# Kernel optimization log

Measured on AMD Instinct MI355X. Metric: run time of the kernel, lower is better.

The kernel has to match this reference:

```python
import jax, jax.numpy as jnp
import numpy as np

B, T, S, DM, H, HID = 4, 1024, 1024, 1024, 16, 4096
DEPTH = DM // H


def setup_inputs() -> dict:
    key = jax.random.key(0)
    ks = jax.random.split(key, 32)
    n = lambda k, shape, scale=1.0: jax.random.normal(k, shape, dtype=jnp.float32) * scale
    w_scale = 1.0 / np.sqrt(DM)
    inp = {
        "x": n(ks[0], (B, T, DM)),
        "enc_out": n(ks[1], (B, S, DM)),
        # causal mask: 1 where attention is forbidden (TF convention mask*-1e9)
        "look_ahead_mask": jnp.broadcast_to(
            jnp.triu(jnp.ones((T, T), jnp.float32), k=1), (B, 1, T, T)),
        "padding_mask": jnp.zeros((B, 1, 1, S), jnp.float32),
    }
    # self-attention MHA params
    names = ["wq1", "wk1", "wv1", "wo1", "wq2", "wk2", "wv2", "wo2"]
    for i, nm in enumerate(names):
        inp[nm] = n(ks[2 + i], (DM, DM), w_scale)
        inp["b" + nm[1:]] = jnp.zeros((DM,), jnp.float32)
    # FFN
    inp["wh"] = n(ks[10], (DM, HID), w_scale)
    inp["bh"] = jnp.zeros((HID,), jnp.float32)
    inp["wout"] = n(ks[11], (HID, DM), 1.0 / np.sqrt(HID))
    inp["bout"] = jnp.zeros((DM,), jnp.float32)
    for i in (1, 2, 3):
        inp[f"g{i}"] = jnp.ones((DM,), jnp.float32)
        inp[f"be{i}"] = jnp.zeros((DM,), jnp.float32)
    return inp


def _layer_norm(x, gamma, beta, eps=1e-6):
    mean = jnp.mean(x, axis=-1, keepdims=True)
    var = jnp.mean(jnp.square(x - mean), axis=-1, keepdims=True)
    return gamma * (x - mean) * jax.lax.rsqrt(var + eps) + beta


def _mha(q_in, k_in, v_in, mask, wq, bq, wk, bk, wv, bv, wo, bo):
    b = q_in.shape[0]
    split = lambda t: t.reshape(b, -1, H, DEPTH).transpose(0, 2, 1, 3)  # [b,h,s,d]
    Q = split(q_in @ wq + bq)
    K = split(k_in @ wk + bk)
    V = split(v_in @ wv + bv)
    scores = jnp.einsum("bhqd,bhkd->bhqk", Q, K) / jnp.sqrt(jnp.float32(DEPTH))
    scores = scores + mask * (-1e9)
    w = jax.nn.softmax(scores, axis=-1)
    out = jnp.einsum("bhqk,bhkd->bhqd", w, V)
    out = out.transpose(0, 2, 1, 3).reshape(b, -1, DM)
    return out @ wo + bo


def reference(x, enc_out, look_ahead_mask, padding_mask,
              wq1, bq1, wk1, bk1, wv1, bv1, wo1, bo1,
              wq2, bq2, wk2, bk2, wv2, bv2, wo2, bo2,
              wh, bh, wout, bout, g1, be1, g2, be2, g3, be3):
    # self-attention + residual + LN (dropout identity at inference)
    a1 = _mha(x, x, x, look_ahead_mask, wq1, bq1, wk1, bk1, wv1, bv1, wo1, bo1)
    h1 = _layer_norm(a1 + x, g1, be1)
    # cross-attention + residual + LN
    a2 = _mha(h1, enc_out, enc_out, padding_mask,
              wq2, bq2, wk2, bk2, wv2, bv2, wo2, bo2)
    h2 = _layer_norm(a2 + h1, g2, be2)
    # FFN + residual + LN
    f = jax.nn.relu(h2 @ wh + bh) @ wout + bout
    return _layer_norm(f + h2, g3, be3)
```

## Files before the change

### kernel.cpp

```cpp
#include <hip/hip_runtime.h>
#include <hip/hip_bf16.h>

typedef __bf16 bf16;
typedef __bf16 bf16x4 __attribute__((ext_vector_type(4)));
typedef __bf16 bf16x8 __attribute__((ext_vector_type(8)));
typedef float floatx4 __attribute__((ext_vector_type(4)));

#define MFMA16(a, b, c) __builtin_amdgcn_mfma_f32_16x16x32_bf16(a, b, c, 0, 0, 0)

#define BB   4
#define TT   1024
#define SS   1024
#define DMOD 1024
#define NH   16
#define DH   64
#define HID  4096
#define MTOT (BB * TT)

__device__ __forceinline__ float loadf(const bf16* p)  { return (float)*p; }
__device__ __forceinline__ float loadf(const float* p) { return *p; }

__device__ __forceinline__ void gll16(const bf16* g, bf16* l) {
    __builtin_amdgcn_global_load_lds(
        (const __attribute__((address_space(1))) void*)g,
        (__attribute__((address_space(3))) void*)l, 16, 0, 0);
}

__device__ __forceinline__ void xcd_swizzle2d(int& bx, int& by) {
    const int gx  = gridDim.x;
    const int nwg = gx * gridDim.y;
    const int lin = blockIdx.y * gx + blockIdx.x;
    const int q   = nwg >> 3;
    const int swz = (lin & 7) * q + (lin >> 3);
    bx = swz % gx;
    by = swz / gx;
}

struct TBatch { const float* src[8]; bf16* dst[8]; };

__global__ __launch_bounds__(256)
void transpose_sq_kernel(TBatch tb)
{
    __shared__ float t[64][65];
    const float* W = tb.src[blockIdx.z];
    bf16* WT = tb.dst[blockIdx.z];
    const int k0 = blockIdx.y * 64, n0 = blockIdx.x * 64;
    const int tid = threadIdx.x;
    const int r = tid >> 4, c = (tid & 15) * 4;
    #pragma unroll
    for (int i = 0; i < 4; ++i) {
        float4 v = *(const float4*)(W + (size_t)(k0 + i * 16 + r) * DMOD + n0 + c);
        t[i * 16 + r][c + 0] = v.x; t[i * 16 + r][c + 1] = v.y;
        t[i * 16 + r][c + 2] = v.z; t[i * 16 + r][c + 3] = v.w;
    }
    __syncthreads();
    #pragma unroll
    for (int i = 0; i < 4; ++i) {
        int n = i * 16 + r;
        bf16x4 o;
        #pragma unroll
        for (int j = 0; j < 4; ++j) o[j] = (bf16)t[c + j][n];
        *(bf16x4*)(WT + (size_t)(n0 + n) * DMOD + k0 + c) = o;
    }
}

__global__ __launch_bounds__(256)
void transpose_kernel(const float* __restrict__ W, bf16* __restrict__ WT, int K, int N)
{
    __shared__ float t[64][65];
    const int k0 = blockIdx.y * 64, n0 = blockIdx.x * 64;
    const int tid = threadIdx.x;
    const int r = tid >> 4, c = (tid & 15) * 4;
    #pragma unroll
    for (int i = 0; i < 4; ++i) {
        float4 v = *(const float4*)(W + (size_t)(k0 + i * 16 + r) * N + n0 + c);
        t[i * 16 + r][c + 0] = v.x; t[i * 16 + r][c + 1] = v.y;
        t[i * 16 + r][c + 2] = v.z; t[i * 16 + r][c + 3] = v.w;
    }
    __syncthreads();
    #pragma unroll
    for (int i = 0; i < 4; ++i) {
        int n = i * 16 + r;
        bf16x4 o;
        #pragma unroll
        for (int j = 0; j < 4; ++j) o[j] = (bf16)t[c + j][n];
        *(bf16x4*)(WT + (size_t)(n0 + n) * K + k0 + c) = o;
    }
}

__global__ __launch_bounds__(256)
void vtrans_kernel(const bf16* __restrict__ in, int ldi, bf16* __restrict__ out)
{
    __shared__ bf16 t[64][72];
    const int r0 = blockIdx.y * 64;
    const int c0 = blockIdx.x * 64;
    const int tid = threadIdx.x;
    const int rr = tid >> 3;
    const int c8 = (tid & 7) * 8;
    #pragma unroll
    for (int i = 0; i < 2; ++i) {
        int row = i * 32 + rr;
        bf16x8 v = *(const bf16x8*)(in + (size_t)(r0 + row) * ldi + c0 + c8);
        *(bf16x8*)(&t[row][c8]) = v;
    }
    __syncthreads();
    #pragma unroll
    for (int i = 0; i < 2; ++i) {
        int col = i * 32 + rr;
        bf16x8 v;
        #pragma unroll
        for (int j = 0; j < 8; ++j) v[j] = t[c8 + j][col];
        *(bf16x8*)(out + (size_t)(c0 + col) * MTOT + r0 + c8) = v;
    }
}

__global__ __launch_bounds__(256)
void cvt_kernel(const float* __restrict__ in, bf16* __restrict__ out, int n4)
{
    int i = blockIdx.x * 256 + threadIdx.x;
    if (i < n4) {
        float4 v = ((const float4*)in)[i];
        bf16x4 o = { (bf16)v.x, (bf16)v.y, (bf16)v.z, (bf16)v.w };
        ((bf16x4*)out)[i] = o;
    }
}

__global__ __launch_bounds__(256)
void bias_concat_kernel(const float* bq1, const float* bk1, const float* bv1,
                        const float* bk2, const float* bv2, float* __restrict__ biasc)
{
    int i = blockIdx.x * 256 + threadIdx.x;
    float v;
    if      (i < 1024) v = bq1[i];
    else if (i < 2048) v = bk1[i - 1024];
    else if (i < 3072) v = bv1[i - 2048];
    else if (i < 4096) v = bk2[i - 3072];
    else               v = bv2[i - 4096];
    if (i < 5120) biasc[i] = v;
}

template <int EPI, typename TR>
__global__ __launch_bounds__(256, 2)
void gemm_kernel(const bf16* __restrict__ A, int lda, const bf16* __restrict__ B,
                 const float* __restrict__ bias, const TR* __restrict__ resid,
                 bf16* __restrict__ out, int M, int N, int K)
{
    __shared__ bf16 Al[2][128 * 64];
    __shared__ bf16 Bl[2][128 * 64];

    const int tid  = threadIdx.x;
    const int wave = tid >> 6;
    const int lane = tid & 63;
    const int l16  = lane & 15;
    const int quad = lane >> 4;
    int bx, by;
    xcd_swizzle2d(bx, by);
    const int bm   = by * 128;
    const int bn   = bx * 128;
    const int wm   = (wave >> 1) * 64;
    const int wn   = (wave & 1) * 64;
    const int lrow = lane >> 3;
    const int scol = ((lane & 7) ^ lrow) * 8;

    floatx4 acc[4][4] = {};
    const int ntk = K / 64;

    auto STAGE = [&](int kt, int buf) {
        const int k0 = kt * 64;
        #pragma unroll
        for (int i = 0; i < 4; ++i) {
            int r0 = (wave * 4 + i) * 8;
            gll16(A + (size_t)(bm + r0 + lrow) * lda + k0 + scol, &Al[buf][r0 * 64]);
            gll16(B + (size_t)(bn + r0 + lrow) * K   + k0 + scol, &Bl[buf][r0 * 64]);
        }
    };

    auto COMPUTE = [&](int buf) {
        #pragma unroll
        for (int ks = 0; ks < 2; ++ks) {
            bf16x8 af[4], bg[4];
            const int xo = ((ks * 4 + quad) ^ (l16 & 7)) * 8;
            #pragma unroll
            for (int mt = 0; mt < 4; ++mt)
                af[mt] = *(const bf16x8*)(&Al[buf][(wm + mt * 16 + l16) * 64 + xo]);
            #pragma unroll
            for (int nt = 0; nt < 4; ++nt)
                bg[nt] = *(const bf16x8*)(&Bl[buf][(wn + nt * 16 + l16) * 64 + xo]);
            #pragma unroll
            for (int mt = 0; mt < 4; ++mt)
                #pragma unroll
                for (int nt = 0; nt < 4; ++nt)
                    acc[mt][nt] = MFMA16(af[mt], bg[nt], acc[mt][nt]);
        }
    };

    STAGE(0, 0);
    asm volatile("s_waitcnt vmcnt(0)" ::: "memory");
    __builtin_amdgcn_s_barrier();

    int cur = 0;
    for (int t = 0; t < ntk - 1; ++t) {
        STAGE(t + 1, cur ^ 1);
        COMPUTE(cur);
        asm volatile("s_waitcnt vmcnt(0) lgkmcnt(0)" ::: "memory");
        __builtin_amdgcn_s_barrier();
        cur ^= 1;
    }
    COMPUTE(cur);

    #pragma unroll
    for (int mt = 0; mt < 4; ++mt) {
        int row0 = bm + wm + mt * 16 + quad * 4;
        #pragma unroll
        for (int nt = 0; nt < 4; ++nt) {
            int col = bn + wn + nt * 16 + l16;
            float bv = bias[col];
            #pragma unroll
            for (int r = 0; r < 4; ++r) {
                float v = acc[mt][nt][r] + bv;
                size_t idx = (size_t)(row0 + r) * N + col;
                if (EPI == 1) v = fmaxf(v, 0.0f);
                if (EPI == 2) v += loadf(resid + idx);
                out[idx] = (bf16)v;
            }
        }
    }
}

template <int EPI, typename TR>
__global__ __launch_bounds__(256, 3)
void gemm64_kernel(const bf16* __restrict__ A, int lda, const bf16* __restrict__ B,
                   const float* __restrict__ bias, const TR* __restrict__ resid,
                   bf16* __restrict__ out, int M, int N, int K)
{
    __shared__ bf16 Al[2][64 * 64];
    __shared__ bf16 Bl[2][128 * 64];

    const int tid  = threadIdx.x;
    const int wave = tid >> 6;
    const int lane = tid & 63;
    const int l16  = lane & 15;
    const int quad = lane >> 4;
    int bx, by;
    xcd_swizzle2d(bx, by);
    const int bm   = by * 64;
    const int bn   = bx * 128;
    const int wm   = (wave >> 1) * 32;
    const int wn   = (wave & 1) * 64;
    const int lrow = lane >> 3;
    const int scol = ((lane & 7) ^ lrow) * 8;

    floatx4 acc[2][4] = {};
    const int ntk = K / 64;

    auto STAGE = [&](int kt, int buf) {
        const int k0 = kt * 64;
        #pragma unroll
        for (int i = 0; i < 2; ++i) {
            int r0 = wave * 16 + i * 8;
            gll16(A + (size_t)(bm + r0 + lrow) * lda + k0 + scol, &Al[buf][r0 * 64]);
        }
        #pragma unroll
        for (int i = 0; i < 4; ++i) {
            int r0 = (wave * 4 + i) * 8;
            gll16(B + (size_t)(bn + r0 + lrow) * K + k0 + scol, &Bl[buf][r0 * 64]);
        }
    };

    auto COMPUTE = [&](int buf) {
        #pragma unroll
        for (int ks = 0; ks < 2; ++ks) {
            bf16x8 af[2], bg[4];
            const int xo = ((ks * 4 + quad) ^ (l16 & 7)) * 8;
            #pragma unroll
            for (int mt = 0; mt < 2; ++mt)
                af[mt] = *(const bf16x8*)(&Al[buf][(wm + mt * 16 + l16) * 64 + xo]);
            #pragma unroll
            for (int nt = 0; nt < 4; ++nt)
                bg[nt] = *(const bf16x8*)(&Bl[buf][(wn + nt * 16 + l16) * 64 + xo]);
            #pragma unroll
            for (int mt = 0; mt < 2; ++mt)
                #pragma unroll
                for (int nt = 0; nt < 4; ++nt)
                    acc[mt][nt] = MFMA16(af[mt], bg[nt], acc[mt][nt]);
        }
    };

    STAGE(0, 0);
    asm volatile("s_waitcnt vmcnt(0)" ::: "memory");
    __builtin_amdgcn_s_barrier();

    int cur = 0;
    for (int t = 0; t < ntk - 1; ++t) {
        STAGE(t + 1, cur ^ 1);
        COMPUTE(cur);
        asm volatile("s_waitcnt vmcnt(0) lgkmcnt(0)" ::: "memory");
        __builtin_amdgcn_s_barrier();
        cur ^= 1;
    }
    COMPUTE(cur);

    #pragma unroll
    for (int mt = 0; mt < 2; ++mt) {
        int row0 = bm + wm + mt * 16 + quad * 4;
        #pragma unroll
        for (int nt = 0; nt < 4; ++nt) {
            int col = bn + wn + nt * 16 + l16;
            float bv = bias[col];
            #pragma unroll
            for (int r = 0; r < 4; ++r) {
                float v = acc[mt][nt][r] + bv;
                size_t idx = (size_t)(row0 + r) * N + col;
                if (EPI == 1) v = fmaxf(v, 0.0f);
                if (EPI == 2) v += loadf(resid + idx);
                out[idx] = (bf16)v;
            }
        }
    }
}

template <int CAUSAL>
__global__ __launch_bounds__(256, 3)
void attn_kernel(const bf16* __restrict__ Q, int ldq, const bf16* __restrict__ K, int ldk,
                 const bf16* __restrict__ Vt, bf16* __restrict__ O, int ldo)
{
    __shared__ bf16 Kl[2][64 * 64];
    __shared__ bf16 Vl[2][64 * 64];
    __shared__ bf16 Pl[4 * 16 * 72];

    const int tid  = threadIdx.x;
    const int wave = tid >> 6;
    const int lane = tid & 63;
    const int l16  = lane & 15;
    const int quad = lane >> 4;
    int bx, byy, bz;
    {
        const int lin = (blockIdx.z * 16 + blockIdx.y) * 16 + blockIdx.x;
        const int swz = (lin & 7) * 128 + (lin >> 3);
        bx  = swz & 15;
        byy = (swz >> 4) & 15;
        bz  = swz >> 8;
    }
    const int qb   = CAUSAL ? (15 - bx) : bx;
    const int h    = byy;
    const int b    = bz;

    const int qrow0 = b * TT + qb * 64 + wave * 16;
    const int colh  = h * DH;
    const int lr8   = lane >> 3;
    const int lc8s  = ((lane & 7) ^ lr8) * 8;

    bf16x8 qa[2];
    #pragma unroll
    for (int c = 0; c < 2; ++c)
        qa[c] = *(const bf16x8*)(Q + (size_t)(qrow0 + l16) * ldq + colh + c * 32 + quad * 8);

    floatx4 o[5] = {};
    const float C = 0.125f * 1.4426950408889634f;
    bf16x8 onesf;
    {
        bf16 ov = (bf16)((l16 == 0) ? 1.0f : 0.0f);
        #pragma unroll
        for (int j = 0; j < 8; ++j) onesf[j] = ov;
    }

    const int ntiles = CAUSAL ? qb + 1 : (SS / 64);
    bf16* pw = Pl + wave * (16 * 72);

    auto STAGE = [&](int t, int buf) {
        const int kv0 = t * 64;
        #pragma unroll
        for (int i = 0; i < 2; ++i) {
            int r0 = wave * 16 + i * 8;
            gll16(K  + (size_t)(b * SS + kv0 + r0 + lr8) * ldk + colh + lc8s, &Kl[buf][r0 * 64]);
            gll16(Vt + (size_t)(colh + r0 + lr8) * MTOT + b * SS + kv0 + lc8s, &Vl[buf][r0 * 64]);
        }
    };

    auto COMPUTE = [&](int t, int buf) {
        const int xo0 = (quad ^ (l16 & 7)) * 8;
        const int xo1 = ((4 + quad) ^ (l16 & 7)) * 8;

        floatx4 s[4];
        #pragma unroll
        for (int nt = 0; nt < 4; ++nt) {
            bf16x8 kb0 = *(const bf16x8*)(&Kl[buf][(nt * 16 + l16) * 64 + xo0]);
            bf16x8 kb1 = *(const bf16x8*)(&Kl[buf][(nt * 16 + l16) * 64 + xo1]);
            floatx4 z = {};
            z = MFMA16(qa[0], kb0, z);
            z = MFMA16(qa[1], kb1, z);
            s[nt] = z;
        }

        const bool dm = CAUSAL && (t == qb);
        #pragma unroll
        for (int nt = 0; nt < 4; ++nt)
            #pragma unroll
            for (int r = 0; r < 4; ++r) {
                float sv = s[nt][r] * C;
                if (dm) {
                    int qg  = wave * 16 + quad * 4 + r;
                    int kvg = nt * 16 + l16;
                    if (kvg > qg) sv = -1e30f;
                }
                float pv = exp2f(sv);
                pw[(quad * 4 + r) * 72 + nt * 16 + l16] = (bf16)pv;
            }

        bf16x8 pa0 = *(const bf16x8*)(pw + l16 * 72 + quad * 8);
        bf16x8 pa1 = *(const bf16x8*)(pw + l16 * 72 + 32 + quad * 8);
        #pragma unroll
        for (int dt = 0; dt < 4; ++dt) {
            bf16x8 vb0 = *(const bf16x8*)(&Vl[buf][(dt * 16 + l16) * 64 + xo0]);
            bf16x8 vb1 = *(const bf16x8*)(&Vl[buf][(dt * 16 + l16) * 64 + xo1]);
            o[dt] = MFMA16(pa0, vb0, o[dt]);
            o[dt] = MFMA16(pa1, vb1, o[dt]);
        }
        o[4] = MFMA16(pa0, onesf, o[4]);
        o[4] = MFMA16(pa1, onesf, o[4]);
    };

    STAGE(0, 0);
    asm volatile("s_waitcnt vmcnt(0)" ::: "memory");
    __builtin_amdgcn_s_barrier();

    int cur = 0;
    for (int t = 0; t < ntiles - 1; ++t) {
        STAGE(t + 1, cur ^ 1);
        COMPUTE(t, cur);
        asm volatile("s_waitcnt vmcnt(0) lgkmcnt(0)" ::: "memory");
        __builtin_amdgcn_s_barrier();
        cur ^= 1;
    }
    COMPUTE(ntiles - 1, cur);

    #pragma unroll
    for (int r = 0; r < 4; ++r) {
        float lr  = __shfl(o[4][r], (lane & 48));
        float inv = __builtin_amdgcn_rcpf(lr);
        #pragma unroll
        for (int dt = 0; dt < 4; ++dt) {
            float ov = o[dt][r] * inv;
            size_t idx = (size_t)(qrow0 + quad * 4 + r) * ldo + colh + dt * 16 + l16;
            O[idx] = (bf16)ov;
        }
    }
}

template <typename TO>
__global__ __launch_bounds__(256)
void ln_kernel(const bf16* __restrict__ in, const float* __restrict__ g,
               const float* __restrict__ be, TO* __restrict__ out)
{
    const int row = blockIdx.x;
    const int tid = threadIdx.x;
    bf16x4 xv = *(const bf16x4*)(in + (size_t)row * DMOD + tid * 4);
    float x0 = (float)xv[0], x1 = (float)xv[1], x2 = (float)xv[2], x3 = (float)xv[3];

    float s = x0 + x1 + x2 + x3;
    #pragma unroll
    for (int off = 32; off >= 1; off >>= 1) s += __shfl_xor(s, off);
    __shared__ float red1[4];
    __shared__ float red2[4];
    const int wave = tid >> 6;
    if ((tid & 63) == 0) red1[wave] = s;
    __syncthreads();
    float mean = (red1[0] + red1[1] + red1[2] + red1[3]) * (1.0f / DMOD);

    float d0 = x0 - mean, d1 = x1 - mean, d2 = x2 - mean, d3 = x3 - mean;
    float sq = d0 * d0 + d1 * d1 + d2 * d2 + d3 * d3;
    #pragma unroll
    for (int off = 32; off >= 1; off >>= 1) sq += __shfl_xor(sq, off);
    if ((tid & 63) == 0) red2[wave] = sq;
    __syncthreads();
    float var = (red2[0] + red2[1] + red2[2] + red2[3]) * (1.0f / DMOD);
    float rs = rsqrtf(var + 1e-6f);

    int c = tid * 4;
    size_t o0 = (size_t)row * DMOD + c;
    out[o0 + 0] = (TO)(g[c + 0] * d0 * rs + be[c + 0]);
    out[o0 + 1] = (TO)(g[c + 1] * d1 * rs + be[c + 1]);
    out[o0 + 2] = (TO)(g[c + 2] * d2 * rs + be[c + 2]);
    out[o0 + 3] = (TO)(g[c + 3] * d3 * rs + be[c + 3]);
}

extern "C" void kernel_launch(void* const* d_in, const int* in_sizes, int n_in,
                              void* d_out, int out_size, void* d_ws, size_t ws_size,
                              hipStream_t stream)
{
    const float* x   = (const float*)d_in[0];
    const float* enc = (const float*)d_in[1];
    const float* wq1 = (const float*)d_in[4];  const float* bq1 = (const float*)d_in[5];
    const float* wk1 = (const float*)d_in[6];  const float* bk1 = (const float*)d_in[7];
    const float* wv1 = (const float*)d_in[8];  const float* bv1 = (const float*)d_in[9];
    const float* wo1 = (const float*)d_in[10]; const float* bo1 = (const float*)d_in[11];
    const float* wq2 = (const float*)d_in[12]; const float* bq2 = (const float*)d_in[13];
    const float* wk2 = (const float*)d_in[14]; const float* bk2 = (const float*)d_in[15];
    const float* wv2 = (const float*)d_in[16]; const float* bv2 = (const float*)d_in[17];
    const float* wo2 = (const float*)d_in[18]; const float* bo2 = (const float*)d_in[19];
    const float* wh  = (const float*)d_in[20]; const float* bh  = (const float*)d_in[21];
    const float* wou = (const float*)d_in[22]; const float* bou = (const float*)d_in[23];
    const float* g1  = (const float*)d_in[24]; const float* be1 = (const float*)d_in[25];
    const float* g2  = (const float*)d_in[26]; const float* be2 = (const float*)d_in[27];
    const float* g3  = (const float*)d_in[28]; const float* be3 = (const float*)d_in[29];

    const int M = MTOT;
    const size_t MB = 1u << 20;
    dim3 blk(256);

    char* ws = (char*)d_ws;
    bf16*  WT    = (bf16*)(ws);
    float* biasc = (float*)(ws + 8 * MB);
    bf16*  xb    = (bf16*)(ws + 9 * MB);
    bf16*  h1    = (bf16*)(ws + 9 * MB);
    bf16*  tmpb3 = (bf16*)(ws + 9 * MB);
    bf16*  encb  = (bf16*)(ws + 17 * MB);
    bf16*  Vt2   = (bf16*)(ws + 17 * MB);
    bf16*  ffn   = (bf16*)(ws + 17 * MB);
    bf16*  qkv   = (bf16*)(ws + 25 * MB);
    bf16*  kvb   = qkv + (size_t)M * 1024;
    bf16*  tmpb2 = qkv + (size_t)M * 1024;
    bf16*  Vt1   = (bf16*)(ws + 49 * MB);
    bf16*  tmpb1 = (bf16*)(ws + 49 * MB);
    bf16*  h2    = (bf16*)(ws + 49 * MB);

    dim3 gThi(HID / 64, DMOD / 64);
    dim3 gTout(DMOD / 64, HID / 64);
    dim3 gVt(DMOD / 64, M / 64);
    dim3 gQKV(3072 / 128, M / 128);
    dim3 gKV(2048 / 128, M / 128);
    dim3 gN64(DMOD / 128, M / 64);
    dim3 gH(HID / 128, M / 128);
    dim3 gA(TT / 64, NH, BB);
    const size_t W1M = (size_t)1024 * 1024;

    cvt_kernel<<<dim3(M * DMOD / 4 / 256), blk, 0, stream>>>(x, xb, M * DMOD / 4);
    cvt_kernel<<<dim3(M * DMOD / 4 / 256), blk, 0, stream>>>(enc, encb, M * DMOD / 4);
    bias_concat_kernel<<<dim3(20), blk, 0, stream>>>(bq1, bk1, bv1, bk2, bv2, biasc);

    {
        TBatch tb;
        tb.src[0] = wq1; tb.dst[0] = WT + 0 * W1M;
        tb.src[1] = wk1; tb.dst[1] = WT + 1 * W1M;
        tb.src[2] = wv1; tb.dst[2] = WT + 2 * W1M;
        tb.src[3] = wo1; tb.dst[3] = WT + 3 * W1M;
        tb.src[4] = tb.src[5] = tb.src[6] = tb.src[7] = wq1;
        tb.dst[4] = tb.dst[5] = tb.dst[6] = tb.dst[7] = WT;
        dim3 g4(16, 16, 4);
        transpose_sq_kernel<<<g4, blk, 0, stream>>>(tb);
    }

    gemm_kernel<0, bf16><<<gQKV, blk, 0, stream>>>(xb, 1024, WT, biasc, (const bf16*)nullptr,
                                                   qkv, M, 3072, 1024);
    vtrans_kernel<<<gVt, blk, 0, stream>>>(qkv + 2048, 3072, Vt1);
    attn_kernel<1><<<gA, blk, 0, stream>>>(qkv, 3072, qkv + 1024, 3072, Vt1, qkv, 3072);
    gemm64_kernel<2, float><<<gN64, blk, 0, stream>>>(qkv, 3072, WT + 3 * W1M, bo1, x,
                                                      tmpb1, M, 1024, 1024);
    ln_kernel<bf16><<<dim3(M), blk, 0, stream>>>(tmpb1, g1, be1, h1);

    {
        TBatch tb;
        tb.src[0] = wq2; tb.dst[0] = WT + 0 * W1M;
        tb.src[1] = wk2; tb.dst[1] = WT + 1 * W1M;
        tb.src[2] = wv2; tb.dst[2] = WT + 2 * W1M;
        tb.src[3] = wo2; tb.dst[3] = WT + 3 * W1M;
        tb.src[4] = tb.src[5] = tb.src[6] = tb.src[7] = wq2;
        tb.dst[4] = tb.dst[5] = tb.dst[6] = tb.dst[7] = WT;
        dim3 g4(16, 16, 4);
        transpose_sq_kernel<<<g4, blk, 0, stream>>>(tb);
    }

    gemm64_kernel<0, bf16><<<gN64, blk, 0, stream>>>(h1, 1024, WT, bq2, (const bf16*)nullptr,
                                                     qkv, M, 1024, 1024);
    gemm_kernel<0, bf16><<<gKV, blk, 0, stream>>>(encb, 1024, WT + 1 * W1M, biasc + 3072,
                                                  (const bf16*)nullptr, kvb, M, 2048, 1024);
    vtrans_kernel<<<gVt, blk, 0, stream>>>(kvb + 1024, 2048, Vt2);
    attn_kernel<0><<<gA, blk, 0, stream>>>(qkv, 1024, kvb, 2048, Vt2, qkv, 1024);
    gemm64_kernel<2, bf16><<<gN64, blk, 0, stream>>>(qkv, 1024, WT + 3 * W1M, bo2, h1,
                                                     tmpb2, M, 1024, 1024);
    ln_kernel<bf16><<<dim3(M), blk, 0, stream>>>(tmpb2, g2, be2, h2);

    transpose_kernel<<<gThi, blk, 0, stream>>>(wh, WT, DMOD, HID);
    gemm_kernel<1, bf16><<<gH, blk, 0, stream>>>(h2, 1024, WT, bh, (const bf16*)nullptr,
                                                 ffn, M, HID, 1024);
    transpose_kernel<<<gTout, blk, 0, stream>>>(wou, WT, HID, DMOD);
    gemm64_kernel<2, bf16><<<gN64, blk, 0, stream>>>(ffn, 4096, WT, bou, h2,
                                                     tmpb3, M, 1024, 4096);
    ln_kernel<float><<<dim3(M), blk, 0, stream>>>(tmpb3, g3, be3, (float*)d_out);
}
```

Measured before the change: 521.8 us.

## Add 256x256-tile 8-wave GEMM with phased prefetch for wide-N projections

```diff
diff --git a/kernel.cpp b/kernel.cpp
--- a/kernel.cpp
+++ b/kernel.cpp
@@ -137,6 +137,155 @@
     else if (i < 4096) v = bk2[i - 3072];
     else               v = bv2[i - 4096];
     if (i < 5120) biasc[i] = v;
+}
+
+template <int EPI, typename TR>
+__global__ __launch_bounds__(512, 2)
+void gemm256_kernel(const bf16* __restrict__ A, int lda, const bf16* __restrict__ B,
+                    const float* __restrict__ bias, const TR* __restrict__ resid,
+                    bf16* __restrict__ out, int M, int N, int K)
+{
+    __shared__ bf16 Al[2][256 * 64];
+    __shared__ bf16 Bl[2][256 * 64];
+
+    const int tid  = threadIdx.x;
+    const int wave = tid >> 6;
+    const int lane = tid & 63;
+    const int l16  = lane & 15;
+    const int quad = lane >> 4;
+    const int wr   = wave >> 2;
+    const int wc   = wave & 3;
+    int bx, by;
+    xcd_swizzle2d(bx, by);
+    const int bm   = by * 256;
+    const int bn   = bx * 256;
+    const int lrow = lane >> 3;
+    const int scol = ((lane & 7) ^ lrow) * 8;
+
+    floatx4 acc[8][4] = {};
+    const int ntk = K / 64;
+
+    auto STAGE_A = [&](int kt, int half, int buf) {
+        const int k0 = kt * 64;
+        #pragma unroll
+        for (int i = 0; i < 2; ++i) {
+            int r0 = half * 128 + i * 64 + wave * 8;
+            gll16(A + (size_t)(bm + r0 + lrow) * lda + k0 + scol, &Al[buf][r0 * 64]);
+        }
+    };
+    auto STAGE_B = [&](int kt, int half, int buf) {
+        const int k0 = kt * 64;
+        #pragma unroll
+        for (int i = 0; i < 2; ++i) {
+            int r0 = half * 128 + i * 64 + wave * 8;
+            gll16(B + (size_t)(bn + r0 + lrow) * K + k0 + scol, &Bl[buf][r0 * 64]);
+        }
+    };
+
+    STAGE_A(0, 0, 0); STAGE_A(0, 1, 0); STAGE_B(0, 0, 0); STAGE_B(0, 1, 0);
+
+    for (int t = 0; t < ntk; ++t) {
+        const int buf = t & 1, nb = buf ^ 1;
+        const bool hn = (t + 1 < ntk);
+        bf16x8 bg[4], af[4];
+
+        if (hn) {
+            STAGE_A(t + 1, 0, nb);
+            asm volatile("s_waitcnt vmcnt(2)" ::: "memory");
+        } else {
+            asm volatile("s_waitcnt vmcnt(0)" ::: "memory");
+        }
+        __builtin_amdgcn_s_barrier();
+        {
+            const int xo = (quad ^ (l16 & 7)) * 8;
+            #pragma unroll
+            for (int i = 0; i < 4; ++i)
+                af[i] = *(const bf16x8*)(&Al[buf][(wr * 128 + i * 16 + l16) * 64 + xo]);
+            #pragma unroll
+            for (int n = 0; n < 4; ++n)
+                bg[n] = *(const bf16x8*)(&Bl[buf][(wc * 64 + n * 16 + l16) * 64 + xo]);
+        }
+        __builtin_amdgcn_s_setprio(1);
+        #pragma unroll
+        for (int i = 0; i < 4; ++i)
+            #pragma unroll
+            for (int n = 0; n < 4; ++n)
+                acc[i][n] = MFMA16(af[i], bg[n], acc[i][n]);
+        __builtin_amdgcn_s_setprio(0);
+        __builtin_amdgcn_s_barrier();
+
+        {
+            const int xo = (quad ^ (l16 & 7)) * 8;
+            #pragma unroll
+            for (int i = 0; i < 4; ++i)
+                af[i] = *(const bf16x8*)(&Al[buf][(wr * 128 + 64 + i * 16 + l16) * 64 + xo]);
+        }
+        if (hn) STAGE_A(t + 1, 1, nb);
+        __builtin_amdgcn_s_barrier();
+        __builtin_amdgcn_s_setprio(1);
+        #pragma unroll
+        for (int i = 0; i < 4; ++i)
+            #pragma unroll
+            for (int n = 0; n < 4; ++n)
+                acc[4 + i][n] = MFMA16(af[i], bg[n], acc[4 + i][n]);
+        __builtin_amdgcn_s_setprio(0);
+        __builtin_amdgcn_s_barrier();
+
+        {
+            const int xo = ((4 + quad) ^ (l16 & 7)) * 8;
+            #pragma unroll
+            for (int i = 0; i < 4; ++i)
+                af[i] = *(const bf16x8*)(&Al[buf][(wr * 128 + i * 16 + l16) * 64 + xo]);
+            #pragma unroll
+            for (int n = 0; n < 4; ++n)
+                bg[n] = *(const bf16x8*)(&Bl[buf][(wc * 64 + n * 16 + l16) * 64 + xo]);
+        }
+        if (hn) STAGE_B(t + 1, 0, nb);
+        __builtin_amdgcn_s_barrier();
+        __builtin_amdgcn_s_setprio(1);
+        #pragma unroll
+        for (int i = 0; i < 4; ++i)
+            #pragma unroll
+            for (int n = 0; n < 4; ++n)
+                acc[i][n] = MFMA16(af[i], bg[n], acc[i][n]);
+        __builtin_amdgcn_s_setprio(0);
+        __builtin_amdgcn_s_barrier();
+
+        {
+            const int xo = ((4 + quad) ^ (l16 & 7)) * 8;
+            #pragma unroll
+            for (int i = 0; i < 4; ++i)
+                af[i] = *(const bf16x8*)(&Al[buf][(wr * 128 + 64 + i * 16 + l16) * 64 + xo]);
+        }
+        if (hn) STAGE_B(t + 1, 1, nb);
+        __builtin_amdgcn_s_barrier();
+        __builtin_amdgcn_s_setprio(1);
+        #pragma unroll
+        for (int i = 0; i < 4; ++i)
+            #pragma unroll
+            for (int n = 0; n < 4; ++n)
+                acc[4 + i][n] = MFMA16(af[i], bg[n], acc[4 + i][n]);
+        __builtin_amdgcn_s_setprio(0);
+        __builtin_amdgcn_s_barrier();
+    }
+
+    #pragma unroll
+    for (int mf = 0; mf < 8; ++mf) {
+        int row0 = bm + wr * 128 + mf * 16 + quad * 4;
+        #pragma unroll
+        for (int nf = 0; nf < 4; ++nf) {
+            int col = bn + wc * 64 + nf * 16 + l16;
+            float bv = bias[col];
+            #pragma unroll
+            for (int r = 0; r < 4; ++r) {
+                float v = acc[mf][nf][r] + bv;
+                size_t idx = (size_t)(row0 + r) * N + col;
+                if (EPI == 1) v = fmaxf(v, 0.0f);
+                if (EPI == 2) v += loadf(resid + idx);
+                out[idx] = (bf16)v;
+            }
+        }
+    }
 }
 
 template <int EPI, typename TR>
@@ -228,7 +377,7 @@
 }
 
 template <int EPI, typename TR>
-__global__ __launch_bounds__(256, 3)
+__global__ __launch_bounds__(256, 2)
 void gemm64_kernel(const bf16* __restrict__ A, int lda, const bf16* __restrict__ B,
                    const float* __restrict__ bias, const TR* __restrict__ resid,
                    bf16* __restrict__ out, int M, int N, int K)
@@ -507,6 +656,7 @@
     const int M = MTOT;
     const size_t MB = 1u << 20;
     dim3 blk(256);
+    dim3 blk512(512);
 
     char* ws = (char*)d_ws;
     bf16*  WT    = (bf16*)(ws);
@@ -527,10 +677,10 @@
     dim3 gThi(HID / 64, DMOD / 64);
     dim3 gTout(DMOD / 64, HID / 64);
     dim3 gVt(DMOD / 64, M / 64);
-    dim3 gQKV(3072 / 128, M / 128);
-    dim3 gKV(2048 / 128, M / 128);
+    dim3 gQKV256(3072 / 256, M / 256);
+    dim3 gKV256(2048 / 256, M / 256);
+    dim3 gFFN1(HID / 256, M / 256);
     dim3 gN64(DMOD / 128, M / 64);
-    dim3 gH(HID / 128, M / 128);
     dim3 gA(TT / 64, NH, BB);
     const size_t W1M = (size_t)1024 * 1024;
 
@@ -550,8 +700,8 @@
         transpose_sq_kernel<<<g4, blk, 0, stream>>>(tb);
     }
 
-    gemm_kernel<0, bf16><<<gQKV, blk, 0, stream>>>(xb, 1024, WT, biasc, (const bf16*)nullptr,
-                                                   qkv, M, 3072, 1024);
+    gemm256_kernel<0, bf16><<<gQKV256, blk512, 0, stream>>>(xb, 1024, WT, biasc,
+                                                            (const bf16*)nullptr, qkv, M, 3072, 1024);
     vtrans_kernel<<<gVt, blk, 0, stream>>>(qkv + 2048, 3072, Vt1);
     attn_kernel<1><<<gA, blk, 0, stream>>>(qkv, 3072, qkv + 1024, 3072, Vt1, qkv, 3072);
     gemm64_kernel<2, float><<<gN64, blk, 0, stream>>>(qkv, 3072, WT + 3 * W1M, bo1, x,
@@ -572,8 +722,8 @@
 
     gemm64_kernel<0, bf16><<<gN64, blk, 0, stream>>>(h1, 1024, WT, bq2, (const bf16*)nullptr,
                                                      qkv, M, 1024, 1024);
-    gemm_kernel<0, bf16><<<gKV, blk, 0, stream>>>(encb, 1024, WT + 1 * W1M, biasc + 3072,
-                                                  (const bf16*)nullptr, kvb, M, 2048, 1024);
+    gemm256_kernel<0, bf16><<<gKV256, blk512, 0, stream>>>(encb, 1024, WT + 1 * W1M, biasc + 3072,
+                                                           (const bf16*)nullptr, kvb, M, 2048, 1024);
     vtrans_kernel<<<gVt, blk, 0, stream>>>(kvb + 1024, 2048, Vt2);
     attn_kernel<0><<<gA, blk, 0, stream>>>(qkv, 1024, kvb, 2048, Vt2, qkv, 1024);
     gemm64_kernel<2, bf16><<<gN64, blk, 0, stream>>>(qkv, 1024, WT + 3 * W1M, bo2, h1,
@@ -581,8 +731,8 @@
     ln_kernel<bf16><<<dim3(M), blk, 0, stream>>>(tmpb2, g2, be2, h2);
 
     transpose_kernel<<<gThi, blk, 0, stream>>>(wh, WT, DMOD, HID);
-    gemm_kernel<1, bf16><<<gH, blk, 0, stream>>>(h2, 1024, WT, bh, (const bf16*)nullptr,
-                                                 ffn, M, HID, 1024);
+    gemm256_kernel<1, bf16><<<gFFN1, blk512, 0, stream>>>(h2, 1024, WT, bh,
+                                                          (const bf16*)nullptr, ffn, M, HID, 1024);
     transpose_kernel<<<gTout, blk, 0, stream>>>(wou, WT, HID, DMOD);
     gemm64_kernel<2, bf16><<<gN64, blk, 0, stream>>>(ffn, 4096, WT, bou, h2,
                                                      tmpb3, M, 1024, 4096);
```

Result: no change. 529.9 us (+1.6%).
